# Kernel optimization log

Measured on AMD Instinct MI355X. Metric: run time of the kernel, lower is better.

Reference implementation:

```python
import jax, jax.numpy as jnp
import numpy as np

N, D, H, E, K = 8192, 1024, 2048, 8, 2

def setup_inputs() -> dict:
    key = jax.random.key(0)
    ks = jax.random.split(key, 8)
    x = jax.random.normal(ks[0], (N, D), dtype=jnp.float32)
    # Expert params stacked over the expert axis (E, ...)
    W1 = jax.random.normal(ks[1], (E, D, H), dtype=jnp.float32) * (1.0 / np.sqrt(D))
    b1 = jnp.zeros((E, H), dtype=jnp.float32)
    W2 = jax.random.normal(ks[2], (E, H, D), dtype=jnp.float32) * (1.0 / np.sqrt(H))
    b2 = jnp.zeros((E, D), dtype=jnp.float32)
    # Gating linear
    Wg = jax.random.normal(ks[3], (D, E), dtype=jnp.float32) * (1.0 / np.sqrt(D))
    bg = jnp.zeros((E,), dtype=jnp.float32)
    # Externalized gating noise (torch uses randn_like(logits) * 0.1)
    noise = jax.random.normal(ks[4], (N, E), dtype=jnp.float32)
    return {"x": x, "W1": W1, "b1": b1, "W2": W2, "b2": b2, "Wg": Wg, "bg": bg, "noise": noise}


def reference(x, W1, b1, W2, b2, Wg, bg, noise):
    n = x.shape[0]
    # --- gating: noisy top-k + softmax over top-k, scattered to dense weights ---
    logits = x @ Wg + bg                                  # [N, E]
    noisy = logits + 0.1 * noise
    top_v, top_i = jax.lax.top_k(noisy, K)                # [N, K]
    w = jax.nn.softmax(top_v, axis=-1)                    # [N, K]
    rows = jnp.arange(n)[:, None]
    sparse_w = jnp.zeros_like(logits).at[rows, top_i].set(w)  # [N, E]
    # --- all experts on all tokens (faithful to the dense-stack implementation) ---
    h = jax.nn.relu(jnp.einsum('nd,edh->neh', x, W1) + b1)    # [N, E, H]
    expert_out = jnp.einsum('neh,ehd->ned', h, W2) + b2       # [N, E, D]
    # --- weighted combine ---
    return jnp.einsum('ne,ned->nd', sparse_w, expert_out)     # [N, D]
```

## Files before the change

### kernel.cpp

```cpp
#include <hip/hip_runtime.h>
#include <stdint.h>
#include <stddef.h>

#define NTOK 8192
#define DDIM 1024
#define HDIM 2048
#define NEXP 8

typedef __attribute__((ext_vector_type(8))) short short8;
typedef __attribute__((ext_vector_type(8))) unsigned short ushort8;
typedef __attribute__((ext_vector_type(4))) float floatx4;

#define AS1 __attribute__((address_space(1)))
#define AS3 __attribute__((address_space(3)))

#define MAXRT 136
#define MAXT1 (MAXRT * (HDIM / 128))
#define MAXT2 (MAXRT * (DDIM / 128))

constexpr size_t OFF_CNT  = 0;
constexpr size_t OFF_TB1  = 256;
constexpr size_t OFF_TB2  = OFF_TB1 + 8960;
constexpr size_t OFF_TKI  = OFF_TB2 + 4608;
constexpr size_t OFF_TKW  = OFF_TKI + (size_t)NTOK * 8;
constexpr size_t OFF_LIST = OFF_TKW + (size_t)NTOK * 8;
constexpr size_t OFF_WTS  = OFF_LIST + (size_t)NEXP * NTOK * 4;
constexpr size_t OFF_XBF  = OFF_WTS + (size_t)NEXP * NTOK * 4;
constexpr size_t OFF_W1T  = OFF_XBF + (size_t)NTOK * DDIM * 2;
constexpr size_t OFF_W2T  = OFF_W1T + (size_t)NEXP * DDIM * HDIM * 2;
constexpr size_t OFF_H    = OFF_W2T + (size_t)NEXP * DDIM * HDIM * 2;

__device__ __forceinline__ unsigned short f2bf(float f) {
  union { float f; unsigned u; } v; v.f = f;
  unsigned r = v.u + 0x7FFFu + ((v.u >> 16) & 1u);
  return (unsigned short)(r >> 16);
}

__global__ __launch_bounds__(256) void gate_kernel(
    const float* __restrict__ x, const float* __restrict__ Wg,
    const float* __restrict__ bg, const float* __restrict__ noise,
    int2* __restrict__ tki, float2* __restrict__ tkw,
    unsigned short* __restrict__ xbf) {
  int lane = threadIdx.x & 63;
  int wid  = threadIdx.x >> 6;
  int token = blockIdx.x * 4 + wid;
  const float* xr = x + (size_t)token * DDIM;
  unsigned short* xo = xbf + (size_t)token * DDIM;
  double acc[NEXP];
#pragma unroll
  for (int e = 0; e < NEXP; ++e) acc[e] = 0.0;
  for (int d = lane; d < DDIM; d += 64) {
    float xv = xr[d];
    xo[d] = f2bf(xv);
    const floatx4* wp = (const floatx4*)(Wg + d * NEXP);
    floatx4 w0 = wp[0], w1 = wp[1];
#pragma unroll
    for (int j = 0; j < 4; ++j) {
      acc[j]     += (double)xv * (double)w0[j];
      acc[4 + j] += (double)xv * (double)w1[j];
    }
  }
#pragma unroll
  for (int e = 0; e < NEXP; ++e)
#pragma unroll
    for (int off = 32; off > 0; off >>= 1) acc[e] += __shfl_xor(acc[e], off);
  if (lane == 0) {
    float nv[NEXP];
#pragma unroll
    for (int e = 0; e < NEXP; ++e) {
      float lg = (float)(acc[e] + (double)bg[e]);
      nv[e] = lg + 0.1f * noise[token * NEXP + e];
    }
    int i1 = 0; float v1 = nv[0];
#pragma unroll
    for (int e = 1; e < NEXP; ++e) if (nv[e] > v1) { v1 = nv[e]; i1 = e; }
    int i2 = -1; float v2 = -3.4e38f;
#pragma unroll
    for (int e = 0; e < NEXP; ++e) if (e != i1 && nv[e] > v2) { v2 = nv[e]; i2 = e; }
    float tt  = expf(v2 - v1);
    tki[token] = make_int2(i1, i2);
    tkw[token] = make_float2(1.0f / (1.0f + tt), tt / (1.0f + tt));
  }
}

__global__ __launch_bounds__(256) void scatter_kernel(
    const int2* __restrict__ tki, const float2* __restrict__ tkw,
    int* __restrict__ counts, int* __restrict__ lists, float* __restrict__ wts) {
  int e = blockIdx.x;
  int tid = threadIdx.x;
  int lane = tid & 63, wid = tid >> 6;
  __shared__ int wave_cnt[4];
  __shared__ int run_total;
  if (tid == 0) run_total = 0;
  __syncthreads();
  for (int t0 = 0; t0 < NTOK; t0 += 256) {
    int tok = t0 + tid;
    int2 ki = tki[tok];
    float2 kw = tkw[tok];
    bool sel = (ki.x == e) || (ki.y == e);
    float w = (ki.x == e) ? kw.x : kw.y;
    unsigned long long mask = __ballot(sel);
    int pos = __popcll(mask & ((1ull << lane) - 1ull));
    if (lane == 0) wave_cnt[wid] = __popcll(mask);
    __syncthreads();
    int base = run_total;
    for (int i = 0; i < wid; ++i) base += wave_cnt[i];
    if (sel) {
      lists[e * NTOK + base + pos] = tok;
      wts[e * NTOK + base + pos] = w;
    }
    __syncthreads();
    if (tid == 0) run_total += wave_cnt[0] + wave_cnt[1] + wave_cnt[2] + wave_cnt[3];
    __syncthreads();
  }
  if (tid == 0) counts[e] = run_total;
}

__global__ __launch_bounds__(256) void build_tiles_kernel(
    const int* __restrict__ counts, int* __restrict__ tb1, int* __restrict__ tb2) {
  int tid = threadIdx.x;
  int ct[8], cum[9];
  cum[0] = 0;
#pragma unroll
  for (int e = 0; e < 8; ++e) { ct[e] = (counts[e] + 127) >> 7; cum[e + 1] = cum[e] + ct[e]; }
  int nt = cum[8];
  constexpr int NBY1 = HDIM / 128, NBY2 = DDIM / 128;
  if (tid == 0) { tb1[0] = nt * NBY1; tb2[0] = nt * NBY2; }
  for (int idx = tid; idx < nt * NBY1; idx += 256) {
    int e = 0;
    while (idx >= cum[e + 1] * NBY1) ++e;
    int r = idx - cum[e] * NBY1;
    int by = r / ct[e], bx = r - by * ct[e];
    tb1[1 + idx] = (e << 16) | (bx << 8) | by;
  }
  for (int idx = tid; idx < nt * NBY2; idx += 256) {
    int e = 0;
    while (idx >= cum[e + 1] * NBY2) ++e;
    int r = idx - cum[e] * NBY2;
    int by = r / ct[e], bx = r - by * ct[e];
    tb2[1 + idx] = (e << 16) | (bx << 8) | by;
  }
}

__global__ __launch_bounds__(256) void transpose_cvt_kernel(
    const float* __restrict__ W, unsigned short* __restrict__ WT, int R, int C) {
  __shared__ float tile[64][65];
  int e = blockIdx.z;
  const float* Win = W + (size_t)e * R * C;
  unsigned short* Wout = WT + (size_t)e * R * C;
  int c0 = blockIdx.x * 64, r0 = blockIdx.y * 64;
  int tx = threadIdx.x & 63, ty = threadIdx.x >> 6;
#pragma unroll
  for (int i = ty; i < 64; i += 4)
    tile[i][tx] = Win[(size_t)(r0 + i) * C + c0 + tx];
  __syncthreads();
  int cc = threadIdx.x >> 2, seg = (threadIdx.x & 3) * 16;
  ushort8 o0, o1;
#pragma unroll
  for (int j = 0; j < 8; ++j) o0[j] = f2bf(tile[seg + j][cc]);
#pragma unroll
  for (int j = 0; j < 8; ++j) o1[j] = f2bf(tile[seg + 8 + j][cc]);
  unsigned short* outp = Wout + (size_t)(c0 + cc) * R + r0 + seg;
  *(ushort8*)(outp) = o0;
  *(ushort8*)(outp + 8) = o1;
}

template <int KDIM, int NDIM, bool IS_G1>
__global__ __launch_bounds__(256) void moe_gemm_kernel(
    const unsigned short* __restrict__ Abase,
    const unsigned short* __restrict__ Bbase,
    const float* __restrict__ bias,
    const int* __restrict__ counts, const int* __restrict__ lists,
    const float* __restrict__ wts, const int* __restrict__ tbl,
    unsigned short* __restrict__ Hout, float* __restrict__ Out) {
  __shared__ __align__(16) char smem[49152];
  constexpr int NT = KDIM / 32;

  int ntiles = tbl[0];
  int bid = blockIdx.x;
  if (bid >= ntiles) return;
  int q = ntiles >> 3, rr = ntiles & 7;
  int xcd = bid & 7, within = bid >> 3;
  int widx = (xcd < rr ? xcd * (q + 1) : rr * (q + 1) + (xcd - rr) * q) + within;
  int desc = tbl[1 + widx];
  int e  = desc >> 16;
  int bx = (desc >> 8) & 0xff;
  int by = desc & 0xff;

  int Me, off_e = 0;
  {
    int c[8];
#pragma unroll
    for (int i = 0; i < 8; ++i) c[i] = counts[i];
    Me = c[e];
#pragma unroll
    for (int i = 0; i < 8; ++i) if (i < e) off_e += c[i];
  }

  int tid = threadIdx.x;
  int lane = tid & 63, wid = tid >> 6;
  int wr = wid >> 1, wc = wid & 1;
  int r16 = lane & 15, g4 = lane >> 4;

  int r0 = tid >> 2;
  int ch = ((tid & 3) ^ ((r0 >> 1) & 3)) * 8;
  const unsigned short *sA0, *sA1, *sB0, *sB1;
  {
    int lr0 = bx * 128 + r0, lr1 = lr0 + 64;
    if (IS_G1) {
      int tk0 = lists[e * NTOK + (lr0 < Me ? lr0 : 0)];
      int tk1 = lists[e * NTOK + (lr1 < Me ? lr1 : 0)];
      sA0 = Abase + (size_t)tk0 * KDIM + ch;
      sA1 = Abase + (size_t)tk1 * KDIM + ch;
    } else {
      sA0 = Abase + (size_t)(off_e + (lr0 < Me ? lr0 : 0)) * KDIM + ch;
      sA1 = Abase + (size_t)(off_e + (lr1 < Me ? lr1 : 0)) * KDIM + ch;
    }
    sB0 = Bbase + ((size_t)e * NDIM + by * 128 + r0) * KDIM + ch;
    sB1 = sB0 + (size_t)64 * KDIM;
  }

  auto stage = [&](int t) {
    int buf = t % 3;
    size_t ko = (size_t)t * 32;
    char* da = smem + buf * 8192 + tid * 16;
    char* db = smem + 24576 + buf * 8192 + tid * 16;
    __builtin_amdgcn_global_load_lds((const AS1 void*)(sA0 + ko), (AS3 void*)da, 16, 0, 0);
    __builtin_amdgcn_global_load_lds((const AS1 void*)(sA1 + ko), (AS3 void*)(da + 4096), 16, 0, 0);
    __builtin_amdgcn_global_load_lds((const AS1 void*)(sB0 + ko), (AS3 void*)db, 16, 0, 0);
    __builtin_amdgcn_global_load_lds((const AS1 void*)(sB1 + ko), (AS3 void*)(db + 4096), 16, 0, 0);
  };

  int aoff[4], boff[4];
#pragma unroll
  for (int m = 0; m < 4; ++m) {
    int rowa = wr * 64 + m * 16 + r16;
    aoff[m] = rowa * 64 + ((g4 ^ ((rowa >> 1) & 3)) * 16);
  }
#pragma unroll
  for (int n = 0; n < 4; ++n) {
    int rowb = wc * 64 + n * 16 + r16;
    boff[n] = 24576 + rowb * 64 + ((g4 ^ ((rowb >> 1) & 3)) * 16);
  }

  floatx4 acc[4][4];
#pragma unroll
  for (int m = 0; m < 4; ++m)
#pragma unroll
    for (int n = 0; n < 4; ++n) acc[m][n] = (floatx4){0.f, 0.f, 0.f, 0.f};

  stage(0);
  stage(1);
  stage(2);

  for (int t = 0; t < NT; ++t) {
    if (t + 2 < NT)      { asm volatile("s_waitcnt vmcnt(8)" ::: "memory"); }
    else if (t + 1 < NT) { asm volatile("s_waitcnt vmcnt(4)" ::: "memory"); }
    else                 { asm volatile("s_waitcnt vmcnt(0)" ::: "memory"); }
    __builtin_amdgcn_s_barrier();
    __builtin_amdgcn_sched_barrier(0);
    const char* pa = smem + (t % 3) * 8192;
    const char* pb = smem + (t % 3) * 8192;
    short8 a[4], b[4];
#pragma unroll
    for (int m = 0; m < 4; ++m) a[m] = *(const short8*)(pa + aoff[m]);
#pragma unroll
    for (int n = 0; n < 4; ++n) b[n] = *(const short8*)(pb + boff[n]);
    __builtin_amdgcn_s_setprio(1);
#pragma unroll
    for (int m = 0; m < 4; ++m)
#pragma unroll
      for (int n = 0; n < 4; ++n)
        acc[m][n] = __builtin_amdgcn_mfma_f32_16x16x32_bf16(a[m], b[n], acc[m][n], 0, 0, 0);
    __builtin_amdgcn_s_setprio(0);
    __builtin_amdgcn_s_barrier();
    __builtin_amdgcn_sched_barrier(0);
    if (t + 3 < NT) stage(t + 3);
  }

  if constexpr (IS_G1) {
#pragma unroll
    for (int m = 0; m < 4; ++m) {
#pragma unroll
      for (int i = 0; i < 4; ++i) {
        int lrow = bx * 128 + wr * 64 + m * 16 + g4 * 4 + i;
        if (lrow < Me) {
          size_t hbase = (size_t)(off_e + lrow) * NDIM + by * 128;
#pragma unroll
          for (int n = 0; n < 4; ++n) {
            int col = wc * 64 + n * 16 + r16;
            float v = acc[m][n][i] + bias[e * NDIM + by * 128 + col];
            Hout[hbase + col] = f2bf(fmaxf(v, 0.f));
          }
        }
      }
    }
  } else {
#pragma unroll
    for (int m = 0; m < 4; ++m) {
#pragma unroll
      for (int i = 0; i < 4; ++i) {
        int lrow = bx * 128 + wr * 64 + m * 16 + g4 * 4 + i;
        if (lrow < Me) {
          int tok = lists[e * NTOK + lrow];
          float w = wts[e * NTOK + lrow];
          float* orow = Out + (size_t)tok * NDIM + by * 128;
#pragma unroll
          for (int n = 0; n < 4; ++n) {
            int col = wc * 64 + n * 16 + r16;
            float v = acc[m][n][i] + bias[e * NDIM + by * 128 + col];
            atomicAdd(orow + col, w * v);
          }
        }
      }
    }
  }
}

extern "C" void kernel_launch(void* const* d_in, const int* in_sizes, int n_in,
                              void* d_out, int out_size, void* d_ws, size_t ws_size,
                              hipStream_t stream) {
  (void)in_sizes; (void)n_in; (void)ws_size;
  const float* x     = (const float*)d_in[0];
  const float* W1    = (const float*)d_in[1];
  const float* b1    = (const float*)d_in[2];
  const float* W2    = (const float*)d_in[3];
  const float* b2    = (const float*)d_in[4];
  const float* Wg    = (const float*)d_in[5];
  const float* bg    = (const float*)d_in[6];
  const float* noise = (const float*)d_in[7];
  float* out = (float*)d_out;

  char* ws = (char*)d_ws;
  int*            counts = (int*)(ws + OFF_CNT);
  int*            tb1    = (int*)(ws + OFF_TB1);
  int*            tb2    = (int*)(ws + OFF_TB2);
  int2*           tki    = (int2*)(ws + OFF_TKI);
  float2*         tkw    = (float2*)(ws + OFF_TKW);
  int*            lists  = (int*)(ws + OFF_LIST);
  float*          wts    = (float*)(ws + OFF_WTS);
  unsigned short* xbf    = (unsigned short*)(ws + OFF_XBF);
  unsigned short* w1t    = (unsigned short*)(ws + OFF_W1T);
  unsigned short* w2t    = (unsigned short*)(ws + OFF_W2T);
  unsigned short* h      = (unsigned short*)(ws + OFF_H);

  hipMemsetAsync(d_out, 0, (size_t)out_size * sizeof(float), stream);
  hipMemsetAsync(counts, 0, 256, stream);

  gate_kernel<<<NTOK / 4, 256, 0, stream>>>(x, Wg, bg, noise, tki, tkw, xbf);
  scatter_kernel<<<NEXP, 256, 0, stream>>>(tki, tkw, counts, lists, wts);
  build_tiles_kernel<<<1, 256, 0, stream>>>(counts, tb1, tb2);
  transpose_cvt_kernel<<<dim3(HDIM / 64, DDIM / 64, NEXP), 256, 0, stream>>>(W1, w1t, DDIM, HDIM);
  transpose_cvt_kernel<<<dim3(DDIM / 64, HDIM / 64, NEXP), 256, 0, stream>>>(W2, w2t, HDIM, DDIM);

  moe_gemm_kernel<DDIM, HDIM, true>
      <<<MAXT1, 256, 0, stream>>>(xbf, w1t, b1, counts, lists, wts, tb1, h, nullptr);
  moe_gemm_kernel<HDIM, DDIM, false>
      <<<MAXT2, 256, 0, stream>>>(h, w2t, b2, counts, lists, wts, tb2, nullptr, out);
}
```

Before: 372.8 us.

## Double K-step to 64 with double-buffered LDS and 8-way swizzle

The MoE GEMM kernel now advances K by 64 per iteration instead of 32. It switches from a triple-buffered to a double-buffered LDS ring (64KB) and uses an 8-chunk XOR swizzle on 128-byte rows. This halves the number of barriers and waitcnt points per tile and issues 8 async global-to-LDS loads per stage. The trade-off is one less stage of prefetch depth and a larger LDS footprint, which may limit blocks per CU.

```diff
diff --git a/kernel.cpp b/kernel.cpp
--- a/kernel.cpp
+++ b/kernel.cpp
@@ -173,8 +173,8 @@
     const int* __restrict__ counts, const int* __restrict__ lists,
     const float* __restrict__ wts, const int* __restrict__ tbl,
     unsigned short* __restrict__ Hout, float* __restrict__ Out) {
-  __shared__ __align__(16) char smem[49152];
-  constexpr int NT = KDIM / 32;
+  __shared__ __align__(16) char smem[65536];
+  constexpr int NT = KDIM / 64;
 
   int ntiles = tbl[0];
   int bid = blockIdx.x;
@@ -202,45 +202,43 @@
   int wr = wid >> 1, wc = wid & 1;
   int r16 = lane & 15, g4 = lane >> 4;
 
-  int r0 = tid >> 2;
-  int ch = ((tid & 3) ^ ((r0 >> 1) & 3)) * 8;
-  const unsigned short *sA0, *sA1, *sB0, *sB1;
-  {
-    int lr0 = bx * 128 + r0, lr1 = lr0 + 64;
+  int r0 = tid >> 3;
+  int ch = ((tid & 7) ^ (r0 & 7)) * 8;
+  const unsigned short *sA[4], *sB[4];
+#pragma unroll
+  for (int i = 0; i < 4; ++i) {
+    int lr = bx * 128 + i * 32 + r0;
     if (IS_G1) {
-      int tk0 = lists[e * NTOK + (lr0 < Me ? lr0 : 0)];
-      int tk1 = lists[e * NTOK + (lr1 < Me ? lr1 : 0)];
-      sA0 = Abase + (size_t)tk0 * KDIM + ch;
-      sA1 = Abase + (size_t)tk1 * KDIM + ch;
+      int tk = lists[e * NTOK + (lr < Me ? lr : 0)];
+      sA[i] = Abase + (size_t)tk * KDIM + ch;
     } else {
-      sA0 = Abase + (size_t)(off_e + (lr0 < Me ? lr0 : 0)) * KDIM + ch;
-      sA1 = Abase + (size_t)(off_e + (lr1 < Me ? lr1 : 0)) * KDIM + ch;
-    }
-    sB0 = Bbase + ((size_t)e * NDIM + by * 128 + r0) * KDIM + ch;
-    sB1 = sB0 + (size_t)64 * KDIM;
+      sA[i] = Abase + (size_t)(off_e + (lr < Me ? lr : 0)) * KDIM + ch;
+    }
+    sB[i] = Bbase + ((size_t)e * NDIM + by * 128 + i * 32 + r0) * KDIM + ch;
   }
 
   auto stage = [&](int t) {
-    int buf = t % 3;
-    size_t ko = (size_t)t * 32;
-    char* da = smem + buf * 8192 + tid * 16;
-    char* db = smem + 24576 + buf * 8192 + tid * 16;
-    __builtin_amdgcn_global_load_lds((const AS1 void*)(sA0 + ko), (AS3 void*)da, 16, 0, 0);
-    __builtin_amdgcn_global_load_lds((const AS1 void*)(sA1 + ko), (AS3 void*)(da + 4096), 16, 0, 0);
-    __builtin_amdgcn_global_load_lds((const AS1 void*)(sB0 + ko), (AS3 void*)db, 16, 0, 0);
-    __builtin_amdgcn_global_load_lds((const AS1 void*)(sB1 + ko), (AS3 void*)(db + 4096), 16, 0, 0);
+    int buf = t & 1;
+    size_t ko = (size_t)t * 64;
+    char* da = smem + buf * 16384 + (tid >> 3) * 128 + (tid & 7) * 16;
+    char* db = da + 32768;
+#pragma unroll
+    for (int i = 0; i < 4; ++i) {
+      __builtin_amdgcn_global_load_lds((const AS1 void*)(sA[i] + ko), (AS3 void*)(da + i * 4096), 16, 0, 0);
+      __builtin_amdgcn_global_load_lds((const AS1 void*)(sB[i] + ko), (AS3 void*)(db + i * 4096), 16, 0, 0);
+    }
   };
 
-  int aoff[4], boff[4];
+  int aoff[4][2], boff[4][2];
 #pragma unroll
   for (int m = 0; m < 4; ++m) {
     int rowa = wr * 64 + m * 16 + r16;
-    aoff[m] = rowa * 64 + ((g4 ^ ((rowa >> 1) & 3)) * 16);
-  }
-#pragma unroll
-  for (int n = 0; n < 4; ++n) {
-    int rowb = wc * 64 + n * 16 + r16;
-    boff[n] = 24576 + rowb * 64 + ((g4 ^ ((rowb >> 1) & 3)) * 16);
+    int rowb = wc * 64 + m * 16 + r16;
+#pragma unroll
+    for (int kk = 0; kk < 2; ++kk) {
+      aoff[m][kk] = rowa * 128 + (((kk * 4 + g4) ^ (rowa & 7)) * 16);
+      boff[m][kk] = 32768 + rowb * 128 + (((kk * 4 + g4) ^ (rowb & 7)) * 16);
+    }
   }
 
   floatx4 acc[4][4];
@@ -251,31 +249,33 @@
 
   stage(0);
   stage(1);
-  stage(2);
 
   for (int t = 0; t < NT; ++t) {
-    if (t + 2 < NT)      { asm volatile("s_waitcnt vmcnt(8)" ::: "memory"); }
-    else if (t + 1 < NT) { asm volatile("s_waitcnt vmcnt(4)" ::: "memory"); }
-    else                 { asm volatile("s_waitcnt vmcnt(0)" ::: "memory"); }
+    if (t + 1 < NT) { asm volatile("s_waitcnt vmcnt(8)" ::: "memory"); }
+    else            { asm volatile("s_waitcnt vmcnt(0)" ::: "memory"); }
     __builtin_amdgcn_s_barrier();
     __builtin_amdgcn_sched_barrier(0);
-    const char* pa = smem + (t % 3) * 8192;
-    const char* pb = smem + (t % 3) * 8192;
-    short8 a[4], b[4];
-#pragma unroll
-    for (int m = 0; m < 4; ++m) a[m] = *(const short8*)(pa + aoff[m]);
-#pragma unroll
-    for (int n = 0; n < 4; ++n) b[n] = *(const short8*)(pb + boff[n]);
+    const char* p = smem + (t & 1) * 16384;
+    short8 a[4][2], b[4][2];
+#pragma unroll
+    for (int m = 0; m < 4; ++m)
+#pragma unroll
+      for (int kk = 0; kk < 2; ++kk) {
+        a[m][kk] = *(const short8*)(p + aoff[m][kk]);
+        b[m][kk] = *(const short8*)(p + boff[m][kk]);
+      }
     __builtin_amdgcn_s_setprio(1);
 #pragma unroll
-    for (int m = 0; m < 4; ++m)
-#pragma unroll
-      for (int n = 0; n < 4; ++n)
-        acc[m][n] = __builtin_amdgcn_mfma_f32_16x16x32_bf16(a[m], b[n], acc[m][n], 0, 0, 0);
+    for (int kk = 0; kk < 2; ++kk)
+#pragma unroll
+      for (int m = 0; m < 4; ++m)
+#pragma unroll
+        for (int n = 0; n < 4; ++n)
+          acc[m][n] = __builtin_amdgcn_mfma_f32_16x16x32_bf16(a[m][kk], b[n][kk], acc[m][n], 0, 0, 0);
     __builtin_amdgcn_s_setprio(0);
     __builtin_amdgcn_s_barrier();
     __builtin_amdgcn_sched_barrier(0);
-    if (t + 3 < NT) stage(t + 3);
+    if (t + 2 < NT) stage(t + 2);
   }
 
   if constexpr (IS_G1) {
```

New measurement: 394.0 us. 1.06x slower.

## Enlarge MoE GEMM tiles to 256x256 with 512-thread blocks

Applied to the files above, without the earlier changes.

Both expert GEMMs now use 256x256 output tiles computed by 8 waves in a 2x4 layout, each wave covering 128x64 with 8x4 MFMA accumulators. LDS triple buffers double to 96KB, and tile tables, workspace offsets and grid sizes are resized to match. The aim is more data reuse per global load and fewer redundant A/B fetches. In exchange there are fewer blocks, likely one per CU, more padding waste on partly filled expert row tiles, and higher register pressure.

```diff
diff --git a/kernel.cpp b/kernel.cpp
--- a/kernel.cpp
+++ b/kernel.cpp
@@ -14,14 +14,13 @@
 #define AS1 __attribute__((address_space(1)))
 #define AS3 __attribute__((address_space(3)))
 
-#define MAXRT 136
-#define MAXT1 (MAXRT * (HDIM / 128))
-#define MAXT2 (MAXRT * (DDIM / 128))
+#define MAXT1 (72 * (HDIM / 256))
+#define MAXT2 (72 * (DDIM / 256))
 
 constexpr size_t OFF_CNT  = 0;
 constexpr size_t OFF_TB1  = 256;
-constexpr size_t OFF_TB2  = OFF_TB1 + 8960;
-constexpr size_t OFF_TKI  = OFF_TB2 + 4608;
+constexpr size_t OFF_TB2  = OFF_TB1 + 4096;
+constexpr size_t OFF_TKI  = OFF_TB2 + 2048;
 constexpr size_t OFF_TKW  = OFF_TKI + (size_t)NTOK * 8;
 constexpr size_t OFF_LIST = OFF_TKW + (size_t)NTOK * 8;
 constexpr size_t OFF_WTS  = OFF_LIST + (size_t)NEXP * NTOK * 4;
@@ -122,9 +121,9 @@
   int ct[8], cum[9];
   cum[0] = 0;
 #pragma unroll
-  for (int e = 0; e < 8; ++e) { ct[e] = (counts[e] + 127) >> 7; cum[e + 1] = cum[e] + ct[e]; }
+  for (int e = 0; e < 8; ++e) { ct[e] = (counts[e] + 255) >> 8; cum[e + 1] = cum[e] + ct[e]; }
   int nt = cum[8];
-  constexpr int NBY1 = HDIM / 128, NBY2 = DDIM / 128;
+  constexpr int NBY1 = HDIM / 256, NBY2 = DDIM / 256;
   if (tid == 0) { tb1[0] = nt * NBY1; tb2[0] = nt * NBY2; }
   for (int idx = tid; idx < nt * NBY1; idx += 256) {
     int e = 0;
@@ -166,14 +165,14 @@
 }
 
 template <int KDIM, int NDIM, bool IS_G1>
-__global__ __launch_bounds__(256) void moe_gemm_kernel(
+__global__ __launch_bounds__(512) void moe_gemm_kernel(
     const unsigned short* __restrict__ Abase,
     const unsigned short* __restrict__ Bbase,
     const float* __restrict__ bias,
     const int* __restrict__ counts, const int* __restrict__ lists,
     const float* __restrict__ wts, const int* __restrict__ tbl,
     unsigned short* __restrict__ Hout, float* __restrict__ Out) {
-  __shared__ __align__(16) char smem[49152];
+  __shared__ __align__(16) char smem[98304];
   constexpr int NT = KDIM / 32;
 
   int ntiles = tbl[0];
@@ -199,53 +198,51 @@
 
   int tid = threadIdx.x;
   int lane = tid & 63, wid = tid >> 6;
-  int wr = wid >> 1, wc = wid & 1;
+  int wr = wid >> 2, wc = wid & 3;
   int r16 = lane & 15, g4 = lane >> 4;
 
   int r0 = tid >> 2;
-  int ch = ((tid & 3) ^ ((r0 >> 1) & 3)) * 8;
-  const unsigned short *sA0, *sA1, *sB0, *sB1;
-  {
-    int lr0 = bx * 128 + r0, lr1 = lr0 + 64;
+  int ch = ((tid & 3) ^ ((tid >> 3) & 3)) * 8;
+  const unsigned short *sA[2], *sB[2];
+#pragma unroll
+  for (int i = 0; i < 2; ++i) {
+    int lr = bx * 256 + i * 128 + r0;
     if (IS_G1) {
-      int tk0 = lists[e * NTOK + (lr0 < Me ? lr0 : 0)];
-      int tk1 = lists[e * NTOK + (lr1 < Me ? lr1 : 0)];
-      sA0 = Abase + (size_t)tk0 * KDIM + ch;
-      sA1 = Abase + (size_t)tk1 * KDIM + ch;
+      int tk = lists[e * NTOK + (lr < Me ? lr : 0)];
+      sA[i] = Abase + (size_t)tk * KDIM + ch;
     } else {
-      sA0 = Abase + (size_t)(off_e + (lr0 < Me ? lr0 : 0)) * KDIM + ch;
-      sA1 = Abase + (size_t)(off_e + (lr1 < Me ? lr1 : 0)) * KDIM + ch;
-    }
-    sB0 = Bbase + ((size_t)e * NDIM + by * 128 + r0) * KDIM + ch;
-    sB1 = sB0 + (size_t)64 * KDIM;
+      sA[i] = Abase + (size_t)(off_e + (lr < Me ? lr : 0)) * KDIM + ch;
+    }
+    sB[i] = Bbase + ((size_t)e * NDIM + by * 256 + i * 128 + r0) * KDIM + ch;
   }
 
   auto stage = [&](int t) {
     int buf = t % 3;
     size_t ko = (size_t)t * 32;
-    char* da = smem + buf * 8192 + tid * 16;
-    char* db = smem + 24576 + buf * 8192 + tid * 16;
-    __builtin_amdgcn_global_load_lds((const AS1 void*)(sA0 + ko), (AS3 void*)da, 16, 0, 0);
-    __builtin_amdgcn_global_load_lds((const AS1 void*)(sA1 + ko), (AS3 void*)(da + 4096), 16, 0, 0);
-    __builtin_amdgcn_global_load_lds((const AS1 void*)(sB0 + ko), (AS3 void*)db, 16, 0, 0);
-    __builtin_amdgcn_global_load_lds((const AS1 void*)(sB1 + ko), (AS3 void*)(db + 4096), 16, 0, 0);
+    char* da = smem + buf * 16384 + tid * 16;
+    char* db = smem + 49152 + buf * 16384 + tid * 16;
+#pragma unroll
+    for (int i = 0; i < 2; ++i) {
+      __builtin_amdgcn_global_load_lds((const AS1 void*)(sA[i] + ko), (AS3 void*)(da + i * 8192), 16, 0, 0);
+      __builtin_amdgcn_global_load_lds((const AS1 void*)(sB[i] + ko), (AS3 void*)(db + i * 8192), 16, 0, 0);
+    }
   };
 
-  int aoff[4], boff[4];
-#pragma unroll
-  for (int m = 0; m < 4; ++m) {
-    int rowa = wr * 64 + m * 16 + r16;
+  int aoff[8], boff[4];
+#pragma unroll
+  for (int m = 0; m < 8; ++m) {
+    int rowa = wr * 128 + m * 16 + r16;
     aoff[m] = rowa * 64 + ((g4 ^ ((rowa >> 1) & 3)) * 16);
   }
 #pragma unroll
   for (int n = 0; n < 4; ++n) {
     int rowb = wc * 64 + n * 16 + r16;
-    boff[n] = 24576 + rowb * 64 + ((g4 ^ ((rowb >> 1) & 3)) * 16);
-  }
-
-  floatx4 acc[4][4];
-#pragma unroll
-  for (int m = 0; m < 4; ++m)
+    boff[n] = 49152 + rowb * 64 + ((g4 ^ ((rowb >> 1) & 3)) * 16);
+  }
+
+  floatx4 acc[8][4];
+#pragma unroll
+  for (int m = 0; m < 8; ++m)
 #pragma unroll
     for (int n = 0; n < 4; ++n) acc[m][n] = (floatx4){0.f, 0.f, 0.f, 0.f};
 
@@ -259,16 +256,15 @@
     else                 { asm volatile("s_waitcnt vmcnt(0)" ::: "memory"); }
     __builtin_amdgcn_s_barrier();
     __builtin_amdgcn_sched_barrier(0);
-    const char* pa = smem + (t % 3) * 8192;
-    const char* pb = smem + (t % 3) * 8192;
-    short8 a[4], b[4];
-#pragma unroll
-    for (int m = 0; m < 4; ++m) a[m] = *(const short8*)(pa + aoff[m]);
-#pragma unroll
-    for (int n = 0; n < 4; ++n) b[n] = *(const short8*)(pb + boff[n]);
+    const char* p = smem + (t % 3) * 16384;
+    short8 a[8], b[4];
+#pragma unroll
+    for (int m = 0; m < 8; ++m) a[m] = *(const short8*)(p + aoff[m]);
+#pragma unroll
+    for (int n = 0; n < 4; ++n) b[n] = *(const short8*)(p + boff[n]);
     __builtin_amdgcn_s_setprio(1);
 #pragma unroll
-    for (int m = 0; m < 4; ++m)
+    for (int m = 0; m < 8; ++m)
 #pragma unroll
       for (int n = 0; n < 4; ++n)
         acc[m][n] = __builtin_amdgcn_mfma_f32_16x16x32_bf16(a[m], b[n], acc[m][n], 0, 0, 0);
@@ -280,16 +276,16 @@
 
   if constexpr (IS_G1) {
 #pragma unroll
-    for (int m = 0; m < 4; ++m) {
+    for (int m = 0; m < 8; ++m) {
 #pragma unroll
       for (int i = 0; i < 4; ++i) {
-        int lrow = bx * 128 + wr * 64 + m * 16 + g4 * 4 + i;
+        int lrow = bx * 256 + wr * 128 + m * 16 + g4 * 4 + i;
         if (lrow < Me) {
-          size_t hbase = (size_t)(off_e + lrow) * NDIM + by * 128;
+          size_t hbase = (size_t)(off_e + lrow) * NDIM + by * 256;
 #pragma unroll
           for (int n = 0; n < 4; ++n) {
             int col = wc * 64 + n * 16 + r16;
-            float v = acc[m][n][i] + bias[e * NDIM + by * 128 + col];
+            float v = acc[m][n][i] + bias[e * NDIM + by * 256 + col];
             Hout[hbase + col] = f2bf(fmaxf(v, 0.f));
           }
         }
@@ -297,18 +293,18 @@
     }
   } else {
 #pragma unroll
-    for (int m = 0; m < 4; ++m) {
+    for (int m = 0; m < 8; ++m) {
 #pragma unroll
       for (int i = 0; i < 4; ++i) {
-        int lrow = bx * 128 + wr * 64 + m * 16 + g4 * 4 + i;
+        int lrow = bx * 256 + wr * 128 + m * 16 + g4 * 4 + i;
         if (lrow < Me) {
           int tok = lists[e * NTOK + lrow];
           float w = wts[e * NTOK + lrow];
-          float* orow = Out + (size_t)tok * NDIM + by * 128;
+          float* orow = Out + (size_t)tok * NDIM + by * 256;
 #pragma unroll
           for (int n = 0; n < 4; ++n) {
             int col = wc * 64 + n * 16 + r16;
-            float v = acc[m][n][i] + bias[e * NDIM + by * 128 + col];
+            float v = acc[m][n][i] + bias[e * NDIM + by * 256 + col];
             atomicAdd(orow + col, w * v);
           }
         }
@@ -354,7 +350,7 @@
   transpose_cvt_kernel<<<dim3(DDIM / 64, HDIM / 64, NEXP), 256, 0, stream>>>(W2, w2t, HDIM, DDIM);
 
   moe_gemm_kernel<DDIM, HDIM, true>
-      <<<MAXT1, 256, 0, stream>>>(xbf, w1t, b1, counts, lists, wts, tb1, h, nullptr);
+      <<<MAXT1, 512, 0, stream>>>(xbf, w1t, b1, counts, lists, wts, tb1, h, nullptr);
   moe_gemm_kernel<HDIM, DDIM, false>
-      <<<MAXT2, 256, 0, stream>>>(h, w2t, b2, counts, lists, wts, tb2, nullptr, out);
-}
+      <<<MAXT2, 512, 0, stream>>>(h, w2t, b2, counts, lists, wts, tb2, nullptr, out);
+}
```

Result: slower. 455.3 us (+22.1%).
